# Kernel tuning notes

Measured on AMD Instinct MI355X. Metric: run time of the kernel, lower is better.

The kernel has to match this reference:

```python
import jax, jax.numpy as jnp
import numpy as np

B, D, T = 8, 256, 8192
N_Q, BINS = 8, 1024
COMMIT_W = 0.25

def setup_inputs() -> dict:
    key = jax.random.key(0)
    k1, k2 = jax.random.split(key)
    x = jax.random.normal(k1, (B, D, T), dtype=jnp.float32)
    codebooks = jax.random.normal(k2, (N_Q, BINS, D), dtype=jnp.float32)
    return {"x": x, "sample_rate": 16000, "codebooks": codebooks}

def _rvq(x_btd, codebooks):
    # x_btd: [B, T, D]; codebooks: [n_q, bins, D]
    def step(residual, cb):
        # nearest codebook entry under squared euclidean distance
        dots = jnp.einsum('btd,kd->btk', residual, cb)          # [B, T, K]
        cb_sq = jnp.sum(cb * cb, axis=-1)                        # [K]
        dist = cb_sq[None, None, :] - 2.0 * dots                 # argmin-equivalent distance
        idx = jnp.argmin(dist, axis=-1)                          # [B, T] int32
        q = cb[idx]                                              # [B, T, D] gather
        # commitment loss (codebook side detached, EnCodec style)
        loss = COMMIT_W * jnp.mean((jax.lax.stop_gradient(q) - residual) ** 2)
        # straight-through estimator
        q_ste = residual + jax.lax.stop_gradient(q - residual)
        return residual - q_ste, (q_ste, idx, loss)

    _, (qs, codes, losses) = jax.lax.scan(step, x_btd, codebooks)
    quantized = jnp.sum(qs, axis=0)                              # [B, T, D]
    return quantized, codes, losses

def reference(x, sample_rate, codebooks):
    n_q = codebooks.shape[0]
    bins = codebooks.shape[1]
    x_btd = jnp.transpose(x, (0, 2, 1))                          # [B, T, D]
    quantized_btd, codes, losses = _rvq(x_btd, codebooks)
    quantized = jnp.transpose(quantized_btd, (0, 2, 1))          # [B, D, T]
    bw_per_q = np.log2(bins) * sample_rate / 1000.0
    bw = jnp.asarray(n_q * bw_per_q, dtype=x.dtype)
    commit_loss = jnp.mean(losses)
    return quantized, codes, bw, commit_loss
```

## Files before the change

### kernel.cpp

```cpp
#include <hip/hip_runtime.h>
#include <math.h>

typedef _Float16 f16;
typedef f16 f16x8 __attribute__((ext_vector_type(8)));
typedef float f32x4 __attribute__((ext_vector_type(4)));

#define B_ 8
#define D_ 256
#define T_ 8192
#define NQ 8
#define KB 1024
#define TT 64
#define NTHR 256
#define SCALE_UP 2048.0f
#define SCALE_DN 4.8828125e-4f

#define OUT_CODES (B_ * D_ * T_)
#define OUT_BW (OUT_CODES + NQ * B_ * T_)
#define OUT_LOSS (OUT_BW + 1)

#define R_BYTES 65536
#define RED_OFF R_BYTES
#define REDI_OFF (RED_OFF + 1024)
#define SEL_OFF (REDI_OFF + 1024)
#define WSUM_OFF (SEL_OFF + 256)
#define LDS_TOTAL (WSUM_OFF + 16)

#define WS_HI (8192 * 4)
#define CBW_HALVES (NQ * 8 * KB * 32)
#define WS_LO (WS_HI + CBW_HALVES * 2)

__global__ void init_cbsq_kernel(const float* __restrict__ cb, const int* __restrict__ sr,
                                 float* __restrict__ csq, float* __restrict__ out) {
    int gid = blockIdx.x * blockDim.x + threadIdx.x;
    int row = gid >> 6;
    int lane = gid & 63;
    float4 v = ((const float4*)(cb + (size_t)row * D_))[lane];
    float s = fmaf(v.x, v.x, fmaf(v.y, v.y, fmaf(v.z, v.z, v.w * v.w)));
#pragma unroll
    for (int off = 32; off; off >>= 1) s += __shfl_down(s, off);
    if (lane == 0) csq[row] = s;
    if (gid == 0) {
        out[OUT_BW] = (float)(*sr) * (80.0f / 1000.0f);
        out[OUT_LOSS] = 0.0f;
    }
}

__global__ void init_split_kernel(const float* __restrict__ cb, f16* __restrict__ whi,
                                  f16* __restrict__ wlo) {
    int gid = blockIdx.x * 256 + threadIdx.x;
    int qdc = gid >> 10, k = gid & 1023;
    int q = qdc >> 3, dc = qdc & 7;
    const float* src = cb + ((size_t)(q * 1024 + k)) * 256 + dc * 32;
    size_t wo = (size_t)gid * 32;
#pragma unroll
    for (int jj = 0; jj < 4; ++jj) {
        float4 a = ((const float4*)src)[jj * 2];
        float4 c = ((const float4*)src)[jj * 2 + 1];
        float vals[8] = {a.x, a.y, a.z, a.w, c.x, c.y, c.z, c.w};
        f16x8 hv, lv;
#pragma unroll
        for (int i = 0; i < 8; ++i) {
            f16 h = (f16)vals[i];
            hv[i] = h;
            lv[i] = (f16)((vals[i] - (float)h) * SCALE_UP);
        }
        *(f16x8*)&whi[wo + jj * 8] = hv;
        *(f16x8*)&wlo[wo + jj * 8] = lv;
    }
}

extern "C" __global__ __launch_bounds__(NTHR, 2)
void rvq_kernel(const float* __restrict__ x, const float* __restrict__ cb,
                const float* __restrict__ csq, const f16* __restrict__ whi,
                const f16* __restrict__ wlo, float* __restrict__ out) {
    extern __shared__ char smem[];
    f16* rs = (f16*)smem;
    float* redv = (float*)(smem + RED_OFF);
    int* redi = (int*)(smem + REDI_OFF);
    int* sel = (int*)(smem + SEL_OFF);
    float* wsum = (float*)(smem + WSUM_OFF);

    const int tid = threadIdx.x;
    const int w = tid >> 6;
    const int l = tid & 63;
    const int l15 = l & 15;
    const int q4 = l >> 4;

    const int b = blockIdx.x >> 7;
    const int t0 = (blockIdx.x & 127) * TT;
    const float* xb = x + (size_t)b * D_ * T_;

    for (int d = tid >> 6; d < D_; d += 4) {
        float v = xb[(size_t)d * T_ + t0 + l];
        f16 h = (f16)v;
        const int sw = l & 7;
        rs[l * 512 + (((d >> 3) ^ sw) << 3) + (d & 7)] = h;
        rs[l * 512 + ((((d >> 3) + 32) ^ sw) << 3) + (d & 7)] = (f16)((v - (float)h) * SCALE_UP);
    }

    float ssq = 0.0f;

    for (int q = 0; q < NQ; ++q) {
        const float* cbq = cb + (size_t)q * KB * D_;
        const char* wq = (const char*)(whi + (size_t)q * 8 * KB * 32);
        const char* lq = (const char*)(wlo + (size_t)q * 8 * KB * 32);

        __syncthreads();

        float bval[16];
        int bidx[16];
#pragma unroll
        for (int e = 0; e < 16; ++e) { bval[e] = INFINITY; bidx[e] = 0; }

        for (int s = 0; s < 4; ++s) {
            int voff[4];
#pragma unroll
            for (int nt = 0; nt < 4; ++nt)
                voff[nt] = (s * 256 + w * 64 + nt * 16 + l15) * 64 + q4 * 16;

            f32x4 ah[4][4], am[4][4];
#pragma unroll
            for (int mt = 0; mt < 4; ++mt)
#pragma unroll
                for (int nt = 0; nt < 4; ++nt) { ah[mt][nt] = (f32x4)0.0f; am[mt][nt] = (f32x4)0.0f; }

            f16x8 cb1[4], cb2[4];
#pragma unroll
            for (int nt = 0; nt < 4; ++nt) {
                cb1[nt] = *(const f16x8*)(wq + voff[nt]);
                cb2[nt] = *(const f16x8*)(lq + voff[nt]);
            }

#pragma unroll 1
            for (int dc = 0; dc < 8; ++dc) {
                f16x8 nb1[4], nb2[4];
                if (dc < 7) {
                    const char* bp1 = wq + (dc + 1) * 65536;
                    const char* bp2 = lq + (dc + 1) * 65536;
#pragma unroll
                    for (int nt = 0; nt < 4; ++nt) {
                        nb1[nt] = *(const f16x8*)(bp1 + voff[nt]);
                        nb2[nt] = *(const f16x8*)(bp2 + voff[nt]);
                    }
                }
                const int ga = dc * 4 + q4;
#pragma unroll
                for (int mt = 0; mt < 4; ++mt) {
                    const int t = mt * 16 + l15;
                    const f16* rowp = rs + t * 512;
                    const int sw = t & 7;
                    f16x8 af1 = *(const f16x8*)&rowp[(ga ^ sw) << 3];
                    f16x8 af2 = *(const f16x8*)&rowp[((ga + 32) ^ sw) << 3];
#pragma unroll
                    for (int nt = 0; nt < 4; ++nt) {
                        ah[mt][nt] = __builtin_amdgcn_mfma_f32_16x16x32_f16(af1, cb1[nt], ah[mt][nt], 0, 0, 0);
                        am[mt][nt] = __builtin_amdgcn_mfma_f32_16x16x32_f16(af2, cb1[nt], am[mt][nt], 0, 0, 0);
                        am[mt][nt] = __builtin_amdgcn_mfma_f32_16x16x32_f16(af1, cb2[nt], am[mt][nt], 0, 0, 0);
                    }
                }
                if (dc < 7) {
#pragma unroll
                    for (int nt = 0; nt < 4; ++nt) { cb1[nt] = nb1[nt]; cb2[nt] = nb2[nt]; }
                }
            }
            const int cbase = s * 256 + w * 64 + l15;
#pragma unroll
            for (int nt = 0; nt < 4; ++nt) {
                const int code = cbase + nt * 16;
                const float cq = csq[q * KB + code];
#pragma unroll
                for (int mt = 0; mt < 4; ++mt)
#pragma unroll
                    for (int rg = 0; rg < 4; ++rg) {
                        const float dot = fmaf(am[mt][nt][rg], SCALE_DN, ah[mt][nt][rg]);
                        const float dist = fmaf(-2.0f, dot, cq);
                        const int e = mt * 4 + rg;
                        if (dist < bval[e]) { bval[e] = dist; bidx[e] = code; }
                    }
            }
        }
#pragma unroll
        for (int m = 1; m < 16; m <<= 1) {
#pragma unroll
            for (int e = 0; e < 16; ++e) {
                const float ov = __shfl_xor(bval[e], m);
                const int oi = __shfl_xor(bidx[e], m);
                if (ov < bval[e] || (ov == bval[e] && oi < bidx[e])) { bval[e] = ov; bidx[e] = oi; }
            }
        }
        if (l15 == 0) {
#pragma unroll
            for (int mt = 0; mt < 4; ++mt)
#pragma unroll
                for (int rg = 0; rg < 4; ++rg) {
                    const int t = mt * 16 + q4 * 4 + rg;
                    redv[w * 64 + t] = bval[mt * 4 + rg];
                    redi[w * 64 + t] = bidx[mt * 4 + rg];
                }
        }
        __syncthreads();
        if (tid < TT) {
            float bv = redv[tid];
            int bi = redi[tid];
#pragma unroll
            for (int w2 = 1; w2 < 4; ++w2) {
                const float v = redv[w2 * 64 + tid];
                const int ii = redi[w2 * 64 + tid];
                if (v < bv || (v == bv && ii < bi)) { bv = v; bi = ii; }
            }
            sel[tid] = bi;
            out[OUT_CODES + ((size_t)q * B_ + b) * T_ + t0 + tid] = (float)bi;
        }
        __syncthreads();
        {
            const int t = tid & 63, ch = tid >> 6;
            const float* crow = cbq + (size_t)sel[t] * D_ + ch * 64;
            f16* rowp = rs + t * 512;
            const int sw = t & 7;
#pragma unroll
            for (int jj = 0; jj < 8; ++jj) {
                const int g1 = ((ch * 8 + jj) ^ sw) << 3;
                const int g2 = ((ch * 8 + jj + 32) ^ sw) << 3;
                f16x8 hv = *(const f16x8*)&rowp[g1];
                f16x8 lv = *(const f16x8*)&rowp[g2];
                const float4 c0 = *(const float4*)&crow[jj * 8];
                const float4 c1 = *(const float4*)&crow[jj * 8 + 4];
                const float cc[8] = {c0.x, c0.y, c0.z, c0.w, c1.x, c1.y, c1.z, c1.w};
                f16x8 nh, nl;
#pragma unroll
                for (int i = 0; i < 8; ++i) {
                    const float r = fmaf((float)lv[i], SCALE_DN, (float)hv[i]);
                    const float nv = r - cc[i];
                    ssq = fmaf(nv, nv, ssq);
                    const f16 h = (f16)nv;
                    nh[i] = h;
                    nl[i] = (f16)((nv - (float)h) * SCALE_UP);
                }
                *(f16x8*)&rowp[g1] = nh;
                *(f16x8*)&rowp[g2] = nl;
            }
        }
    }
    __syncthreads();
    {
        float* outq = out + (size_t)b * D_ * T_;
        for (int d = tid >> 6; d < D_; d += 4) {
            const int sw = l & 7;
            const float h1 = (float)rs[l * 512 + (((d >> 3) ^ sw) << 3) + (d & 7)];
            const float h2 = (float)rs[l * 512 + ((((d >> 3) + 32) ^ sw) << 3) + (d & 7)];
            const size_t gi = (size_t)d * T_ + t0 + l;
            outq[gi] = xb[gi] - fmaf(h2, SCALE_DN, h1);
        }
    }
#pragma unroll
    for (int off = 32; off; off >>= 1) ssq += __shfl_down(ssq, off);
    if (l == 0) wsum[w] = ssq;
    __syncthreads();
    if (tid == 0) {
        const float scale = 0.25f / ((float)NQ * (float)B_ * (float)D_ * (float)T_);
        atomicAdd(out + OUT_LOSS, (wsum[0] + wsum[1] + wsum[2] + wsum[3]) * scale);
    }
}

extern "C" void kernel_launch(void* const* d_in, const int* in_sizes, int n_in,
                              void* d_out, int out_size, void* d_ws, size_t ws_size,
                              hipStream_t stream) {
    const float* x = (const float*)d_in[0];
    const int* sr = (const int*)d_in[1];
    const float* cb = (const float*)d_in[2];
    float* out = (float*)d_out;
    float* csq = (float*)d_ws;
    f16* whi = (f16*)((char*)d_ws + WS_HI);
    f16* wlo = (f16*)((char*)d_ws + WS_LO);

    hipFuncSetAttribute((const void*)rvq_kernel, hipFuncAttributeMaxDynamicSharedMemorySize,
                        LDS_TOTAL);

    init_cbsq_kernel<<<2048, 256, 0, stream>>>(cb, sr, csq, out);
    init_split_kernel<<<256, 256, 0, stream>>>(cb, whi, wlo);
    rvq_kernel<<<B_ * (T_ / TT), NTHR, LDS_TOTAL, stream>>>(x, cb, csq, whi, wlo, out);
}
```

Before: 1.058 ms.

## Split token tile across two wave rows with 512-thread blocks

```diff
diff --git a/kernel.cpp b/kernel.cpp
--- a/kernel.cpp
+++ b/kernel.cpp
@@ -11,7 +11,7 @@
 #define NQ 8
 #define KB 1024
 #define TT 64
-#define NTHR 256
+#define NTHR 512
 #define SCALE_UP 2048.0f
 #define SCALE_DN 4.8828125e-4f
 
@@ -22,9 +22,8 @@
 #define R_BYTES 65536
 #define RED_OFF R_BYTES
 #define REDI_OFF (RED_OFF + 1024)
-#define SEL_OFF (REDI_OFF + 1024)
-#define WSUM_OFF (SEL_OFF + 256)
-#define LDS_TOTAL (WSUM_OFF + 16)
+#define WSUM_OFF (REDI_OFF + 1024)
+#define LDS_TOTAL (WSUM_OFF + 32)
 
 #define WS_HI (8192 * 4)
 #define CBW_HALVES (NQ * 8 * KB * 32)
@@ -70,7 +69,7 @@
     }
 }
 
-extern "C" __global__ __launch_bounds__(NTHR, 2)
+extern "C" __global__ __launch_bounds__(NTHR, 4)
 void rvq_kernel(const float* __restrict__ x, const float* __restrict__ cb,
                 const float* __restrict__ csq, const f16* __restrict__ whi,
                 const f16* __restrict__ wlo, float* __restrict__ out) {
@@ -78,7 +77,6 @@
     f16* rs = (f16*)smem;
     float* redv = (float*)(smem + RED_OFF);
     int* redi = (int*)(smem + REDI_OFF);
-    int* sel = (int*)(smem + SEL_OFF);
     float* wsum = (float*)(smem + WSUM_OFF);
 
     const int tid = threadIdx.x;
@@ -86,12 +84,14 @@
     const int l = tid & 63;
     const int l15 = l & 15;
     const int q4 = l >> 4;
+    const int wm = w >> 2;
+    const int wn = w & 3;
 
     const int b = blockIdx.x >> 7;
     const int t0 = (blockIdx.x & 127) * TT;
     const float* xb = x + (size_t)b * D_ * T_;
 
-    for (int d = tid >> 6; d < D_; d += 4) {
+    for (int d = tid >> 6; d < D_; d += 8) {
         float v = xb[(size_t)d * T_ + t0 + l];
         f16 h = (f16)v;
         const int sw = l & 7;
@@ -108,69 +108,54 @@
 
         __syncthreads();
 
-        float bval[16];
-        int bidx[16];
-#pragma unroll
-        for (int e = 0; e < 16; ++e) { bval[e] = INFINITY; bidx[e] = 0; }
+        float bval[8];
+        int bidx[8];
+#pragma unroll
+        for (int e = 0; e < 8; ++e) { bval[e] = INFINITY; bidx[e] = 0; }
+
+        const int swA = l15 & 7;
 
         for (int s = 0; s < 4; ++s) {
-            int voff[4];
-#pragma unroll
-            for (int nt = 0; nt < 4; ++nt)
-                voff[nt] = (s * 256 + w * 64 + nt * 16 + l15) * 64 + q4 * 16;
-
-            f32x4 ah[4][4], am[4][4];
-#pragma unroll
-            for (int mt = 0; mt < 4; ++mt)
+            const int vbase = ((s * 256 + wn * 64 + l15) << 6) + q4 * 16;
+
+            f32x4 ah[2][4], am[2][4];
+#pragma unroll
+            for (int mt = 0; mt < 2; ++mt)
 #pragma unroll
                 for (int nt = 0; nt < 4; ++nt) { ah[mt][nt] = (f32x4)0.0f; am[mt][nt] = (f32x4)0.0f; }
-
-            f16x8 cb1[4], cb2[4];
-#pragma unroll
-            for (int nt = 0; nt < 4; ++nt) {
-                cb1[nt] = *(const f16x8*)(wq + voff[nt]);
-                cb2[nt] = *(const f16x8*)(lq + voff[nt]);
-            }
 
 #pragma unroll 1
             for (int dc = 0; dc < 8; ++dc) {
-                f16x8 nb1[4], nb2[4];
-                if (dc < 7) {
-                    const char* bp1 = wq + (dc + 1) * 65536;
-                    const char* bp2 = lq + (dc + 1) * 65536;
-#pragma unroll
-                    for (int nt = 0; nt < 4; ++nt) {
-                        nb1[nt] = *(const f16x8*)(bp1 + voff[nt]);
-                        nb2[nt] = *(const f16x8*)(bp2 + voff[nt]);
+                const int ga = dc * 4 + q4;
+                f16x8 af1[2], af2[2];
+#pragma unroll
+                for (int mt = 0; mt < 2; ++mt) {
+                    const f16* rowp = rs + (wm * 32 + mt * 16 + l15) * 512;
+                    af1[mt] = *(const f16x8*)&rowp[(ga ^ swA) << 3];
+                    af2[mt] = *(const f16x8*)&rowp[((ga + 32) ^ swA) << 3];
+                }
+                const char* wqd = wq + dc * 65536;
+                const char* lqd = lq + dc * 65536;
+#pragma unroll
+                for (int nt = 0; nt < 4; ++nt) {
+                    const int off = vbase + nt * 1024;
+                    const f16x8 cb1 = *(const f16x8*)(wqd + off);
+                    const f16x8 cb2 = *(const f16x8*)(lqd + off);
+#pragma unroll
+                    for (int mt = 0; mt < 2; ++mt) {
+                        ah[mt][nt] = __builtin_amdgcn_mfma_f32_16x16x32_f16(af1[mt], cb1, ah[mt][nt], 0, 0, 0);
+                        am[mt][nt] = __builtin_amdgcn_mfma_f32_16x16x32_f16(af2[mt], cb1, am[mt][nt], 0, 0, 0);
+                        am[mt][nt] = __builtin_amdgcn_mfma_f32_16x16x32_f16(af1[mt], cb2, am[mt][nt], 0, 0, 0);
                     }
                 }
-                const int ga = dc * 4 + q4;
-#pragma unroll
-                for (int mt = 0; mt < 4; ++mt) {
-                    const int t = mt * 16 + l15;
-                    const f16* rowp = rs + t * 512;
-                    const int sw = t & 7;
-                    f16x8 af1 = *(const f16x8*)&rowp[(ga ^ sw) << 3];
-                    f16x8 af2 = *(const f16x8*)&rowp[((ga + 32) ^ sw) << 3];
-#pragma unroll
-                    for (int nt = 0; nt < 4; ++nt) {
-                        ah[mt][nt] = __builtin_amdgcn_mfma_f32_16x16x32_f16(af1, cb1[nt], ah[mt][nt], 0, 0, 0);
-                        am[mt][nt] = __builtin_amdgcn_mfma_f32_16x16x32_f16(af2, cb1[nt], am[mt][nt], 0, 0, 0);
-                        am[mt][nt] = __builtin_amdgcn_mfma_f32_16x16x32_f16(af1, cb2[nt], am[mt][nt], 0, 0, 0);
-                    }
-                }
-                if (dc < 7) {
-#pragma unroll
-                    for (int nt = 0; nt < 4; ++nt) { cb1[nt] = nb1[nt]; cb2[nt] = nb2[nt]; }
-                }
-            }
-            const int cbase = s * 256 + w * 64 + l15;
+            }
+            const int cbase = s * 256 + wn * 64 + l15;
 #pragma unroll
             for (int nt = 0; nt < 4; ++nt) {
                 const int code = cbase + nt * 16;
                 const float cq = csq[q * KB + code];
 #pragma unroll
-                for (int mt = 0; mt < 4; ++mt)
+                for (int mt = 0; mt < 2; ++mt)
 #pragma unroll
                     for (int rg = 0; rg < 4; ++rg) {
                         const float dot = fmaf(am[mt][nt][rg], SCALE_DN, ah[mt][nt][rg]);
@@ -183,7 +168,7 @@
 #pragma unroll
         for (int m = 1; m < 16; m <<= 1) {
 #pragma unroll
-            for (int e = 0; e < 16; ++e) {
+            for (int e = 0; e < 8; ++e) {
                 const float ov = __shfl_xor(bval[e], m);
                 const int oi = __shfl_xor(bidx[e], m);
                 if (ov < bval[e] || (ov == bval[e] && oi < bidx[e])) { bval[e] = ov; bidx[e] = oi; }
@@ -191,41 +176,39 @@
         }
         if (l15 == 0) {
 #pragma unroll
-            for (int mt = 0; mt < 4; ++mt)
+            for (int mt = 0; mt < 2; ++mt)
 #pragma unroll
                 for (int rg = 0; rg < 4; ++rg) {
-                    const int t = mt * 16 + q4 * 4 + rg;
-                    redv[w * 64 + t] = bval[mt * 4 + rg];
-                    redi[w * 64 + t] = bidx[mt * 4 + rg];
-                }
-        }
-        __syncthreads();
-        if (tid < TT) {
-            float bv = redv[tid];
-            int bi = redi[tid];
-#pragma unroll
-            for (int w2 = 1; w2 < 4; ++w2) {
-                const float v = redv[w2 * 64 + tid];
-                const int ii = redi[w2 * 64 + tid];
-                if (v < bv || (v == bv && ii < bi)) { bv = v; bi = ii; }
-            }
-            sel[tid] = bi;
-            out[OUT_CODES + ((size_t)q * B_ + b) * T_ + t0 + tid] = (float)bi;
+                    const int tl = mt * 16 + q4 * 4 + rg;
+                    redv[w * 32 + tl] = bval[mt * 4 + rg];
+                    redi[w * 32 + tl] = bidx[mt * 4 + rg];
+                }
         }
         __syncthreads();
         {
             const int t = tid & 63, ch = tid >> 6;
-            const float* crow = cbq + (size_t)sel[t] * D_ + ch * 64;
+            const int wmr = t >> 5, tl = t & 31;
+            float bv = redv[(wmr * 4) * 32 + tl];
+            int bi = redi[(wmr * 4) * 32 + tl];
+#pragma unroll
+            for (int w2 = 1; w2 < 4; ++w2) {
+                const float v = redv[(wmr * 4 + w2) * 32 + tl];
+                const int ii = redi[(wmr * 4 + w2) * 32 + tl];
+                if (v < bv || (v == bv && ii < bi)) { bv = v; bi = ii; }
+            }
+            if (ch == 0) out[OUT_CODES + ((size_t)q * B_ + b) * T_ + t0 + t] = (float)bi;
+            const float* crow = cbq + (size_t)bi * D_ + ch * 32;
             f16* rowp = rs + t * 512;
             const int sw = t & 7;
 #pragma unroll
-            for (int jj = 0; jj < 8; ++jj) {
-                const int g1 = ((ch * 8 + jj) ^ sw) << 3;
-                const int g2 = ((ch * 8 + jj + 32) ^ sw) << 3;
+            for (int jj = 0; jj < 4; ++jj) {
+                const int g = ch * 4 + jj;
+                const int g1 = (g ^ sw) << 3;
+                const int g2 = ((g + 32) ^ sw) << 3;
                 f16x8 hv = *(const f16x8*)&rowp[g1];
                 f16x8 lv = *(const f16x8*)&rowp[g2];
-                const float4 c0 = *(const float4*)&crow[jj * 8];
-                const float4 c1 = *(const float4*)&crow[jj * 8 + 4];
+                const float4 c0 = ((const float4*)crow)[jj * 2];
+                const float4 c1 = ((const float4*)crow)[jj * 2 + 1];
                 const float cc[8] = {c0.x, c0.y, c0.z, c0.w, c1.x, c1.y, c1.z, c1.w};
                 f16x8 nh, nl;
 #pragma unroll
@@ -245,7 +228,7 @@
     __syncthreads();
     {
         float* outq = out + (size_t)b * D_ * T_;
-        for (int d = tid >> 6; d < D_; d += 4) {
+        for (int d = tid >> 6; d < D_; d += 8) {
             const int sw = l & 7;
             const float h1 = (float)rs[l * 512 + (((d >> 3) ^ sw) << 3) + (d & 7)];
             const float h2 = (float)rs[l * 512 + ((((d >> 3) + 32) ^ sw) << 3) + (d & 7)];
@@ -258,8 +241,11 @@
     if (l == 0) wsum[w] = ssq;
     __syncthreads();
     if (tid == 0) {
+        float tot = 0.0f;
+#pragma unroll
+        for (int i = 0; i < 8; ++i) tot += wsum[i];
         const float scale = 0.25f / ((float)NQ * (float)B_ * (float)D_ * (float)T_);
-        atomicAdd(out + OUT_LOSS, (wsum[0] + wsum[1] + wsum[2] + wsum[3]) * scale);
+        atomicAdd(out + OUT_LOSS, tot * scale);
     }
 }
 
```

Result: slower. 3.979 ms (+276.1%).
